# Performance work log

Measured on AMD Instinct MI355X. Metric: run time of the kernel, lower is better.

The kernel has to match this reference:

```python
import jax, jax.numpy as jnp
import numpy as np

EPS = 1e-8  # F.cosine_similarity default eps


def setup_inputs() -> dict:
    key = jax.random.key(0)
    k1, k2, k3, k4 = jax.random.split(key, 4)
    N, M, D, BERT_DIM = 8192, 8192, 128, 768
    return {
        "vision_feature": jax.random.normal(k1, (N, D), dtype=jnp.float32),
        "text_pooled": jax.random.normal(k2, (M, BERT_DIM), dtype=jnp.float32),
        "proj_w": jax.random.normal(k3, (D, BERT_DIM), dtype=jnp.float32) * 0.02,
        "proj_b": jax.random.normal(k4, (D,), dtype=jnp.float32) * 0.02,
    }


def reference(vision_feature, text_pooled, proj_w, proj_b):
    # proj(text_pooled): [M, 768] @ [768, D] + [D] -> [M, D]
    text_feature = text_pooled @ proj_w.T + proj_b
    # Fused cosine similarity: L2-normalize rows (with eps clamp as in
    # F.cosine_similarity), then a single [N,D]x[D,M] GEMM instead of the
    # broadcasted O(N*M*D) intermediate.
    v_norm = jnp.maximum(jnp.linalg.norm(vision_feature, axis=1, keepdims=True), EPS)
    t_norm = jnp.maximum(jnp.linalg.norm(text_feature, axis=1, keepdims=True), EPS)
    vn = vision_feature / v_norm  # [N, D]
    tn = text_feature / t_norm    # [M, D]
    similarity = vn @ tn.T        # [N, M]
    return similarity
```

## Files before the change

kernel.cpp:

```cpp
#include <hip/hip_runtime.h>
#include <stdint.h>

#define NV 8192
#define MT 8192
#define DD 128
#define KB 768

typedef __attribute__((ext_vector_type(8))) short short8;
typedef __attribute__((ext_vector_type(4))) float f32x4;

__device__ __forceinline__ ushort f2bf(float f) {
  uint32_t u = __float_as_uint(f);
  u += 0x7FFF + ((u >> 16) & 1);
  return (ushort)(u >> 16);
}

__global__ __launch_bounds__(256) void k_visnorm(const float* __restrict__ vis,
                                                 ushort* __restrict__ vn) {
  const int tx = threadIdx.x & 15;
  const int r  = blockIdx.x * 16 + (threadIdx.x >> 4);
  const float* p = vis + (size_t)r * DD + tx * 8;
  float4 a = *(const float4*)p;
  float4 b = *(const float4*)(p + 4);
  float s = a.x*a.x + a.y*a.y + a.z*a.z + a.w*a.w
          + b.x*b.x + b.y*b.y + b.z*b.z + b.w*b.w;
  s += __shfl_xor(s, 1, 16);
  s += __shfl_xor(s, 2, 16);
  s += __shfl_xor(s, 4, 16);
  s += __shfl_xor(s, 8, 16);
  const float inv = 1.0f / fmaxf(sqrtf(s), 1e-8f);
  union { ushort u[8]; uint4 v; } o;
  o.u[0] = f2bf(a.x * inv); o.u[1] = f2bf(a.y * inv);
  o.u[2] = f2bf(a.z * inv); o.u[3] = f2bf(a.w * inv);
  o.u[4] = f2bf(b.x * inv); o.u[5] = f2bf(b.y * inv);
  o.u[6] = f2bf(b.z * inv); o.u[7] = f2bf(b.w * inv);
  *(uint4*)(vn + (size_t)r * DD + tx * 8) = o.v;
}

__global__ __launch_bounds__(256) void k_cvt(const float* __restrict__ src,
                                             ushort* __restrict__ dst) {
  const size_t i = ((size_t)blockIdx.x * 256 + threadIdx.x) * 8;
  float4 a = *(const float4*)(src + i);
  float4 b = *(const float4*)(src + i + 4);
  union { ushort u[8]; uint4 v; } o;
  o.u[0] = f2bf(a.x); o.u[1] = f2bf(a.y); o.u[2] = f2bf(a.z); o.u[3] = f2bf(a.w);
  o.u[4] = f2bf(b.x); o.u[5] = f2bf(b.y); o.u[6] = f2bf(b.z); o.u[7] = f2bf(b.w);
  *(uint4*)(dst + i) = o.v;
}

__global__ __launch_bounds__(64) void k_projnorm(const float* __restrict__ txt,
                                                 const ushort* __restrict__ wb,
                                                 const float* __restrict__ bias,
                                                 ushort* __restrict__ tn) {
  const int lane = threadIdx.x;
  const int row0 = blockIdx.x * 16;
  const int lrow = lane & 15;
  const int g    = lane >> 4;
  const int koff = g * 8;

  const float*  ap = txt + (size_t)(row0 + lrow) * KB + koff;
  const ushort* bp = wb + (size_t)lrow * KB + koff;

  f32x4 acc[8] = {};

#pragma unroll 4
  for (int ks = 0; ks < KB / 32; ++ks) {
    float4 f0 = *(const float4*)(ap + ks * 32);
    float4 f1 = *(const float4*)(ap + ks * 32 + 4);
    short8 a;
    a[0] = (short)f2bf(f0.x); a[1] = (short)f2bf(f0.y);
    a[2] = (short)f2bf(f0.z); a[3] = (short)f2bf(f0.w);
    a[4] = (short)f2bf(f1.x); a[5] = (short)f2bf(f1.y);
    a[6] = (short)f2bf(f1.z); a[7] = (short)f2bf(f1.w);
#pragma unroll
    for (int n = 0; n < 8; ++n) {
      short8 b = *(const short8*)(bp + (size_t)n * 16 * KB + ks * 32);
      acc[n] = __builtin_amdgcn_mfma_f32_16x16x32_bf16(a, b, acc[n], 0, 0, 0);
    }
  }

#pragma unroll
  for (int n = 0; n < 8; ++n) {
    float bv = bias[n * 16 + lrow];
#pragma unroll
    for (int j = 0; j < 4; ++j) acc[n][j] += bv;
  }
  float s0 = 0.f, s1 = 0.f, s2 = 0.f, s3 = 0.f;
#pragma unroll
  for (int n = 0; n < 8; ++n) {
    s0 += acc[n][0] * acc[n][0];
    s1 += acc[n][1] * acc[n][1];
    s2 += acc[n][2] * acc[n][2];
    s3 += acc[n][3] * acc[n][3];
  }
#pragma unroll
  for (int d = 1; d < 16; d <<= 1) {
    s0 += __shfl_xor(s0, d, 16);
    s1 += __shfl_xor(s1, d, 16);
    s2 += __shfl_xor(s2, d, 16);
    s3 += __shfl_xor(s3, d, 16);
  }
  float inv[4];
  inv[0] = 1.0f / fmaxf(sqrtf(s0), 1e-8f);
  inv[1] = 1.0f / fmaxf(sqrtf(s1), 1e-8f);
  inv[2] = 1.0f / fmaxf(sqrtf(s2), 1e-8f);
  inv[3] = 1.0f / fmaxf(sqrtf(s3), 1e-8f);

#pragma unroll
  for (int n = 0; n < 8; ++n)
#pragma unroll
    for (int j = 0; j < 4; ++j)
      tn[(size_t)(row0 + g * 4 + j) * DD + n * 16 + lrow] = f2bf(acc[n][j] * inv[j]);
}

__global__ __launch_bounds__(256, 3) void k_sim(const ushort* __restrict__ vn,
                                                const ushort* __restrict__ tn,
                                                float* __restrict__ out) {
  const int lin  = blockIdx.x;
  const int nlin = (lin & 7) * 512 + (lin >> 3);
  const int by   = nlin >> 6;
  const int bx   = nlin & 63;

  const int lane = threadIdx.x & 63;
  const int wave = threadIdx.x >> 6;
  const int row0 = by * 128 + (wave >> 1) * 64;
  const int col0 = bx * 128 + (wave & 1) * 64;
  const int lrow = lane & 15;
  const int kgrp = lane >> 4;

  const ushort* ap = vn + (size_t)(row0 + lrow) * DD + kgrp * 8;
  const ushort* bp = tn + (size_t)(col0 + lrow) * DD + kgrp * 8;

  f32x4 acc[4][4] = {};

#pragma unroll
  for (int ks = 0; ks < 4; ++ks) {
    short8 a[4], b[4];
#pragma unroll
    for (int m = 0; m < 4; ++m)
      a[m] = *(const short8*)(ap + (size_t)m * 16 * DD + ks * 32);
#pragma unroll
    for (int n = 0; n < 4; ++n)
      b[n] = *(const short8*)(bp + (size_t)n * 16 * DD + ks * 32);
#pragma unroll
    for (int m = 0; m < 4; ++m)
#pragma unroll
      for (int n = 0; n < 4; ++n)
        acc[m][n] = __builtin_amdgcn_mfma_f32_16x16x32_bf16(b[n], a[m], acc[m][n], 0, 0, 0);
  }

  float* op = out + (size_t)(row0 + lrow) * MT + col0 + kgrp * 4;
#pragma unroll
  for (int m = 0; m < 4; ++m)
#pragma unroll
    for (int n = 0; n < 4; ++n)
      __builtin_nontemporal_store(acc[m][n],
          (f32x4*)(op + (size_t)m * 16 * MT + n * 16));
}

extern "C" void kernel_launch(void* const* d_in, const int* in_sizes, int n_in,
                              void* d_out, int out_size, void* d_ws, size_t ws_size,
                              hipStream_t stream) {
  (void)in_sizes; (void)n_in; (void)out_size; (void)ws_size;
  const float* vis  = (const float*)d_in[0];
  const float* txt  = (const float*)d_in[1];
  const float* w    = (const float*)d_in[2];
  const float* bias = (const float*)d_in[3];
  float* out = (float*)d_out;

  char* ws = (char*)d_ws;
  ushort* vn = (ushort*)(ws);
  ushort* tn = (ushort*)(ws + (size_t)2097152);
  ushort* wb = (ushort*)(ws + (size_t)4194304);

  k_visnorm<<<NV / 16, 256, 0, stream>>>(vis, vn);
  k_cvt<<<(DD * KB) / 2048, 256, 0, stream>>>(w, wb);
  k_projnorm<<<MT / 16, 64, 0, stream>>>(txt, wb, bias, tn);
  k_sim<<<4096, 256, 0, stream>>>(vn, tn, out);
}
```

Measured before the change: 144.7 us.

## Retile similarity GEMM into per-XCD column slabs with 16x256 wave tiles

Result: slower. 211.3 us (+46.1%).

```diff
diff --git a/kernel.cpp b/kernel.cpp
--- a/kernel.cpp
+++ b/kernel.cpp
@@ -113,49 +113,41 @@
       tn[(size_t)(row0 + g * 4 + j) * DD + n * 16 + lrow] = f2bf(acc[n][j] * inv[j]);
 }
 
-__global__ __launch_bounds__(256, 3) void k_sim(const ushort* __restrict__ vn,
+__global__ __launch_bounds__(512, 4) void k_sim(const ushort* __restrict__ vn,
                                                 const ushort* __restrict__ tn,
                                                 float* __restrict__ out) {
   const int lin  = blockIdx.x;
-  const int nlin = (lin & 7) * 512 + (lin >> 3);
-  const int by   = nlin >> 6;
-  const int bx   = nlin & 63;
+  const int xcd  = lin & 7;
+  const int band = lin >> 3;
+  const int row0 = band * 32;
+  const int colT = xcd * 1024;
 
   const int lane = threadIdx.x & 63;
   const int wave = threadIdx.x >> 6;
-  const int row0 = by * 128 + (wave >> 1) * 64;
-  const int col0 = bx * 128 + (wave & 1) * 64;
+  const int wr   = wave >> 2;
+  const int wc   = wave & 3;
   const int lrow = lane & 15;
   const int kgrp = lane >> 4;
 
-  const ushort* ap = vn + (size_t)(row0 + lrow) * DD + kgrp * 8;
-  const ushort* bp = tn + (size_t)(col0 + lrow) * DD + kgrp * 8;
+  const ushort* ap = vn + (size_t)(row0 + wr * 16 + lrow) * DD + kgrp * 8;
+  const ushort* bp = tn + (size_t)(colT + wc * 256 + lrow) * DD + kgrp * 8;
 
-  f32x4 acc[4][4] = {};
+  f32x4 acc[16] = {};
 
 #pragma unroll
   for (int ks = 0; ks < 4; ++ks) {
-    short8 a[4], b[4];
+    short8 a = *(const short8*)(ap + ks * 32);
 #pragma unroll
-    for (int m = 0; m < 4; ++m)
-      a[m] = *(const short8*)(ap + (size_t)m * 16 * DD + ks * 32);
-#pragma unroll
-    for (int n = 0; n < 4; ++n)
-      b[n] = *(const short8*)(bp + (size_t)n * 16 * DD + ks * 32);
-#pragma unroll
-    for (int m = 0; m < 4; ++m)
-#pragma unroll
-      for (int n = 0; n < 4; ++n)
-        acc[m][n] = __builtin_amdgcn_mfma_f32_16x16x32_bf16(b[n], a[m], acc[m][n], 0, 0, 0);
+    for (int n = 0; n < 16; ++n) {
+      short8 b = *(const short8*)(bp + (size_t)n * 16 * DD + ks * 32);
+      acc[n] = __builtin_amdgcn_mfma_f32_16x16x32_bf16(b, a, acc[n], 0, 0, 0);
+    }
   }
 
-  float* op = out + (size_t)(row0 + lrow) * MT + col0 + kgrp * 4;
+  float* op = out + (size_t)(row0 + wr * 16 + lrow) * MT + colT + wc * 256 + kgrp * 4;
 #pragma unroll
-  for (int m = 0; m < 4; ++m)
-#pragma unroll
-    for (int n = 0; n < 4; ++n)
-      __builtin_nontemporal_store(acc[m][n],
-          (f32x4*)(op + (size_t)m * 16 * MT + n * 16));
+  for (int n = 0; n < 16; ++n)
+    *(f32x4*)(op + n * 16) = acc[n];
 }
 
 extern "C" void kernel_launch(void* const* d_in, const int* in_sizes, int n_in,
@@ -176,5 +168,5 @@
   k_visnorm<<<NV / 16, 256, 0, stream>>>(vis, vn);
   k_cvt<<<(DD * KB) / 2048, 256, 0, stream>>>(w, wb);
   k_projnorm<<<MT / 16, 64, 0, stream>>>(txt, wb, bias, tn);
-  k_sim<<<4096, 256, 0, stream>>>(vn, tn, out);
+  k_sim<<<2048, 512, 0, stream>>>(vn, tn, out);
 }
```
